# Optimization experiments

Hardware: AMD Instinct MI355X
Metric: run time of the kernel (lower is better)

Reference implementation:

```python
import jax, jax.numpy as jnp
import numpy as np

H = 12
DK = 64


def setup_inputs() -> dict:
    key = jax.random.key(0)
    ks = jax.random.split(key, 6)
    bs, ne, d = 32, 20, H * DK
    R = jax.random.normal(ks[0], (bs, ne, ne, d), dtype=jnp.float32)
    R_mas = jax.random.randint(ks[1], (bs, ne, ne, 1), 0, 2).astype(jnp.float32)
    WQ_w = jax.random.normal(ks[2], (DK, DK), dtype=jnp.float32) * (1.0 / np.sqrt(DK))
    WK_w = jax.random.normal(ks[3], (DK, DK), dtype=jnp.float32) * (1.0 / np.sqrt(DK))
    WV_w = jax.random.normal(ks[4], (DK, DK), dtype=jnp.float32) * (1.0 / np.sqrt(DK))
    zb = jnp.zeros((DK,), dtype=jnp.float32)
    return {"R": R, "R_mas": R_mas, "WQ_w": WQ_w, "WQ_b": zb, "WK_w": WK_w,
            "WK_b": zb, "WV_w": WV_w, "WV_b": zb}


def reference(R, R_mas, WQ_w, WQ_b, WK_w, WK_b, WV_w, WV_b):
    bs, ne, _, d = R.shape
    h, dk = H, DK
    n = ne * ne
    # (bs, h, ne, ne, dk)
    Rh = R.reshape(bs, ne, ne, h, dk).transpose(0, 3, 1, 2, 4)
    # per-head QKV linears (torch Linear: y = x @ W.T + b)
    Q = (Rh @ WQ_w.T + WQ_b).reshape(bs, h, n, dk)
    K = (Rh @ WK_w.T + WK_b).reshape(bs, h, n, dk)
    V = (Rh @ WV_w.T + WV_b).reshape(bs, h, n, dk)
    mas = R_mas.reshape(bs, 1, n)                      # (bs,1,n)
    att_mas = mas[:, :, :, None] * mas[:, :, None, :]  # (bs,1,n,n)
    alpha = jnp.einsum('bhqd,bhkd->bhqk', Q, K)        # (bs,h,n,n)
    alpha = alpha - (1.0 - att_mas) * 100000.0         # mask BEFORE scaling (faithful)
    alpha = jax.nn.softmax(alpha / jnp.sqrt(jnp.float32(dk)), axis=-1)
    R_Z = jnp.einsum('bhqk,bhkd->bhqd', alpha, V).reshape(bs, h, ne, ne, dk)
    R_Z = R_Z * R_mas.reshape(bs, 1, ne, ne, 1)
    # (bs, ne, ne, h*dk)
    return R_Z.transpose(0, 2, 3, 1, 4).reshape(bs, ne, ne, h * dk)
```

## Files before the change

kernel.cpp:

```cpp
#include <hip/hip_runtime.h>

typedef float    f32x4 __attribute__((ext_vector_type(4)));
typedef _Float16 f16x8 __attribute__((ext_vector_type(8)));
typedef _Float16 f16x4 __attribute__((ext_vector_type(4)));

#define MFMA16 __builtin_amdgcn_mfma_f32_16x16x32_f16

#define NQ     400
#define DMODEL 768

#define SCL 0.18033688011112042f
#define PEN 18033.688011112043f
#define M0  8.0f

#define K_OFF    0
#define VT_OFF   51200
#define W_OFF    105472
#define QS_OFF   130048
#define BIAS_OFF 162816
#define MKB_OFF  163584
#define SMEM_BYTES 163648

__device__ __forceinline__ f16x8 cvt8(const float* rp) {
    f32x4 u0 = *(const f32x4*)(rp);
    f32x4 u1 = *(const f32x4*)(rp + 4);
    f16x8 a;
    a[0] = (_Float16)u0[0]; a[1] = (_Float16)u0[1];
    a[2] = (_Float16)u0[2]; a[3] = (_Float16)u0[3];
    a[4] = (_Float16)u1[0]; a[5] = (_Float16)u1[1];
    a[6] = (_Float16)u1[2]; a[7] = (_Float16)u1[3];
    return a;
}

template <int M>
__device__ __forceinline__ void proj_kv(char* smem, f16x8 af0, f16x8 af1,
                                        int t, int g, int q16, int csw) {
    #pragma unroll
    for (int cg = 0; cg < 4; ++cg) {
        const int col = cg * 16 + q16;
        const float bb = *(const float*)(smem + BIAS_OFF + (M * 64 + col) * 4);
        f32x4 acc = {bb, bb, bb, bb};
        f16x8 wb0 = *(const f16x8*)(smem + W_OFF + M * 8192 + col * 128 + ((g * 16) ^ csw));
        f16x8 wb1 = *(const f16x8*)(smem + W_OFF + M * 8192 + col * 128 + ((64 + g * 16) ^ csw));
        acc = MFMA16(af0, wb0, acc, 0, 0, 0);
        acc = MFMA16(af1, wb1, acc, 0, 0, 0);
        if (M == 1) {
            #pragma unroll
            for (int r = 0; r < 4; ++r) {
                const int kk = t * 16 + 4 * g + r;
                *(_Float16*)(smem + K_OFF + kk * 128 + ((col * 2) ^ ((kk & 7) << 4))) =
                    (_Float16)acc[r];
            }
        } else {
            f16x4 hv;
            hv[0]=(_Float16)acc[0]; hv[1]=(_Float16)acc[1];
            hv[2]=(_Float16)acc[2]; hv[3]=(_Float16)acc[3];
            *(f16x4*)(smem + VT_OFF + col * 848 + (t >> 1) * 64 + g * 16 + (t & 1) * 8) = hv;
        }
    }
}

__global__ __launch_bounds__(1024, 4)
void attn_fused(const float* __restrict__ R, const float* __restrict__ Rmas,
                const float* __restrict__ Wq, const float* __restrict__ bq,
                const float* __restrict__ Wk, const float* __restrict__ bk,
                const float* __restrict__ Wv, const float* __restrict__ bv,
                float* __restrict__ out)
{
    extern __shared__ char smem[];
    const int tid  = threadIdx.x;
    const int lane = tid & 63;
    const int wv   = tid >> 6;
    const int g    = lane >> 4;
    const int q16  = lane & 15;
    const int csw  = (q16 & 7) << 4;

    const int blk  = blockIdx.x;
    const int b    = blk / 24;
    const int rem  = blk - b * 24;
    const int h    = rem >> 1;
    const int half = rem & 1;
    const int qlo   = half ? 13 : 0;
    const int ntile = half ? 12 : 13;

    {
        if (tid < 768) {
            const int m   = tid >> 8;
            const int idx = tid & 255;
            const int row = idx >> 2;
            const int c0  = (idx & 3) << 4;
            const float* Wm = (m == 0 ? Wq : (m == 1 ? Wk : Wv)) + row * 64 + c0;
            const int sw = (row & 7) << 4;
            #pragma unroll
            for (int k2 = 0; k2 < 2; ++k2) {
                f32x4 v0 = *(const f32x4*)(Wm + 8 * k2);
                f32x4 v1 = *(const f32x4*)(Wm + 8 * k2 + 4);
                f16x8 hv;
                hv[0]=(_Float16)v0[0]; hv[1]=(_Float16)v0[1];
                hv[2]=(_Float16)v0[2]; hv[3]=(_Float16)v0[3];
                hv[4]=(_Float16)v1[0]; hv[5]=(_Float16)v1[1];
                hv[6]=(_Float16)v1[2]; hv[7]=(_Float16)v1[3];
                *(f16x8*)(smem + W_OFF + m * 8192 + row * 128 + ((c0 * 2 + 16 * k2) ^ sw)) = hv;
            }
        } else if (tid < 960) {
            const int j = tid - 768;
            const float* bms[3] = {bq, bk, bv};
            *(float*)(smem + BIAS_OFF + j * 4) = bms[j >> 6][j & 63];
        }
        if (wv < 7) {
            const int i = (wv << 6) | lane;
            const float mval = (i < NQ) ? Rmas[b * NQ + i] : 0.0f;
            unsigned long long bb = __ballot(mval != 0.0f);
            if (lane == 0) {
                ((unsigned*)(smem + MKB_OFF))[2 * wv]     = (unsigned)bb;
                ((unsigned*)(smem + MKB_OFF))[2 * wv + 1] = (unsigned)(bb >> 32);
            }
        }
        if (tid < 256) {
            const int r = tid >> 2, c = tid & 3;
            *(f16x4*)(smem + VT_OFF + r * 848 + 768 + c * 16 + 8) = (f16x4){0, 0, 0, 0};
        }
    }
    __syncthreads();

    const float* Rbh = R + (size_t)b * NQ * DMODEL + h * 64;

    f16x8 qreg[2];
    const int QSw = QS_OFF + wv * 2048;
    if (wv < ntile) {
        const int t = qlo + wv;
        const float* rp = Rbh + (size_t)(t * 16 + q16) * DMODEL + g * 8;
        f16x8 af0 = cvt8(rp);
        f16x8 af1 = cvt8(rp + 32);
        #pragma unroll
        for (int cg = 0; cg < 4; ++cg) {
            const int col = cg * 16 + q16;
            const float bb = *(const float*)(smem + BIAS_OFF + col * 4);
            f32x4 acc = {bb, bb, bb, bb};
            f16x8 wb0 = *(const f16x8*)(smem + W_OFF + col * 128 + ((g * 16) ^ csw));
            f16x8 wb1 = *(const f16x8*)(smem + W_OFF + col * 128 + ((64 + g * 16) ^ csw));
            acc = MFMA16(af0, wb0, acc, 0, 0, 0);
            acc = MFMA16(af1, wb1, acc, 0, 0, 0);
            #pragma unroll
            for (int r = 0; r < 4; ++r) {
                const int rr = 4 * g + r;
                *(_Float16*)(smem + QSw + rr * 128 + ((col * 2) ^ ((rr & 7) << 4))) =
                    (_Float16)acc[r];
            }
        }
        proj_kv<1>(smem, af0, af1, t, g, q16, csw);
        proj_kv<2>(smem, af0, af1, t, g, q16, csw);
        asm volatile("s_waitcnt lgkmcnt(0)" ::: "memory");
        qreg[0] = *(const f16x8*)(smem + QSw + q16 * 128 + ((g * 16)      ^ csw));
        qreg[1] = *(const f16x8*)(smem + QSw + q16 * 128 + ((64 + g * 16) ^ csw));
    }
    {
        const int  t  = half ? (wv - 3) : (9 + wv);
        const bool ok = half ? (wv >= 3) : (wv >= 4);
        if (ok) {
            const float* rp = Rbh + (size_t)(t * 16 + q16) * DMODEL + g * 8;
            f16x8 af0 = cvt8(rp);
            f16x8 af1 = cvt8(rp + 32);
            proj_kv<1>(smem, af0, af1, t, g, q16, csw);
            proj_kv<2>(smem, af0, af1, t, g, q16, csw);
        }
    }
    if (wv == 0) {
        #pragma unroll
        for (int i = 0; i < 7; ++i) {
            const int k = i * 64 + lane;
            if (k < NQ) {
                const unsigned bit =
                    (((const unsigned*)(smem + MKB_OFF))[k >> 5] >> (k & 31)) & 1u;
                *(float*)(smem + QS_OFF + k * 4) = bit ? -M0 : -(M0 + PEN);
            }
        }
    }
    __syncthreads();

    if (wv < ntile) {
        const int qt   = qlo + wv;
        const int qrow = qt * 16 + q16;
        const unsigned qb = (((const unsigned*)(smem + MKB_OFF))[qrow >> 5] >> (qrow & 31)) & 1u;

        const int kbase = K_OFF + q16 * 128;
        const int o0 = (g * 16) ^ csw;
        const int o1 = (64 + g * 16) ^ csw;

        f32x4 oc[4];
        #pragma unroll
        for (int cg = 0; cg < 4; ++cg) oc[cg] = (f32x4){0.f, 0.f, 0.f, 0.f};
        float ps = 0.f;

        f16x8 ka0 = *(const f16x8*)(smem + kbase + o0);
        f16x8 ka1 = *(const f16x8*)(smem + kbase + o1);

        #pragma unroll 1
        for (int kc = 0; kc < 12; ++kc) {
            const char* kb_base = smem + kbase + kc * 4096 + 2048;
            f16x8 kb0 = *(const f16x8*)(kb_base + o0);
            f16x8 kb1 = *(const f16x8*)(kb_base + o1);
            f32x4 pa4 = *(const f32x4*)(smem + QS_OFF + (kc * 32 + 4 * g) * 4);
            f32x4 pb4 = *(const f32x4*)(smem + QS_OFF + (kc * 32 + 16 + 4 * g) * 4);

            f32x4 accA = {0.f, 0.f, 0.f, 0.f};
            accA = MFMA16(ka0, qreg[0], accA, 0, 0, 0);
            accA = MFMA16(ka1, qreg[1], accA, 0, 0, 0);
            f32x4 accB = {0.f, 0.f, 0.f, 0.f};
            accB = MFMA16(kb0, qreg[0], accB, 0, 0, 0);
            accB = MFMA16(kb1, qreg[1], accB, 0, 0, 0);

            const char* kn_base = smem + kbase + (kc + 1) * 4096;
            ka0 = *(const f16x8*)(kn_base + o0);
            ka1 = *(const f16x8*)(kn_base + o1);

            f16x4 pha, phb;
            #pragma unroll
            for (int r = 0; r < 4; ++r) {
                const float e = __builtin_amdgcn_exp2f(fmaf(accA[r], SCL, pa4[r]));
                ps += e;
                pha[r] = (_Float16)e;
            }
            #pragma unroll
            for (int r = 0; r < 4; ++r) {
                const float e = __builtin_amdgcn_exp2f(fmaf(accB[r], SCL, pb4[r]));
                ps += e;
                phb[r] = (_Float16)e;
            }
            union { f16x4 hh[2]; f16x8 v; } pu;
            pu.hh[0] = pha;
            pu.hh[1] = phb;
            const f16x8 pa = pu.v;
            #pragma unroll
            for (int cg = 0; cg < 4; ++cg) {
                f16x8 vb = *(const f16x8*)(smem + VT_OFF + (cg * 16 + q16) * 848 + kc * 64 + g * 16);
                oc[cg] = MFMA16(pa, vb, oc[cg], 0, 0, 0);
            }
        }
        {
            f32x4 pa4 = *(const f32x4*)(smem + QS_OFF + (384 + 4 * g) * 4);
            f32x4 accA = {0.f, 0.f, 0.f, 0.f};
            accA = MFMA16(ka0, qreg[0], accA, 0, 0, 0);
            accA = MFMA16(ka1, qreg[1], accA, 0, 0, 0);
            f16x4 pha;
            #pragma unroll
            for (int r = 0; r < 4; ++r) {
                const float e = __builtin_amdgcn_exp2f(fmaf(accA[r], SCL, pa4[r]));
                ps += e;
                pha[r] = (_Float16)e;
            }
            union { f16x4 hh[2]; f16x8 v; } pu;
            pu.hh[0] = pha;
            pu.hh[1] = (f16x4){0, 0, 0, 0};
            const f16x8 pa = pu.v;
            #pragma unroll
            for (int cg = 0; cg < 4; ++cg) {
                f16x8 vb = *(const f16x8*)(smem + VT_OFF + (cg * 16 + q16) * 848 + 12 * 64 + g * 16);
                oc[cg] = MFMA16(pa, vb, oc[cg], 0, 0, 0);
            }
        }

        ps += __shfl_xor(ps, 16);
        ps += __shfl_xor(ps, 32);
        const float myrs = qb ? __builtin_amdgcn_rcpf(ps) : 0.0f;

        float rs[4];
        #pragma unroll
        for (int r = 0; r < 4; ++r) rs[r] = __shfl(myrs, 4 * g + r);
        float* op = out + (size_t)(b * NQ + qt * 16) * DMODEL + h * 64;
        #pragma unroll
        for (int r = 0; r < 4; ++r) {
            #pragma unroll
            for (int cg = 0; cg < 4; ++cg)
                op[(4 * g + r) * DMODEL + cg * 16 + q16] = oc[cg][r] * rs[r];
        }
    }
}

extern "C" void kernel_launch(void* const* d_in, const int* in_sizes, int n_in,
                              void* d_out, int out_size, void* d_ws, size_t ws_size,
                              hipStream_t stream) {
    const float* R    = (const float*)d_in[0];
    const float* Rmas = (const float*)d_in[1];
    const float* Wq   = (const float*)d_in[2];
    const float* bq   = (const float*)d_in[3];
    const float* Wk   = (const float*)d_in[4];
    const float* bk   = (const float*)d_in[5];
    const float* Wv   = (const float*)d_in[6];
    const float* bv   = (const float*)d_in[7];
    float* out = (float*)d_out;

    (void)hipFuncSetAttribute(reinterpret_cast<const void*>(attn_fused),
                              hipFuncAttributeMaxDynamicSharedMemorySize, SMEM_BYTES);
    attn_fused<<<dim3(768), dim3(1024), SMEM_BYTES, stream>>>(R, Rmas, Wq, bq, Wk, bk, Wv, bv, out);
}
```

Baseline: 49.05 us.

## Compute Q transposed in registers, pack f16 conversions, prefetch K fully

The Q projection now swaps the MFMA operand order so the output lands directly in the register layout the attention loop needs. This removes the Q staging through shared memory and the wait on it. The K projection is transposed the same way so it writes packed f16x4 stores instead of scalar halves. Float-to-half conversions use the packed round-toward-zero instruction, which lowers the conversion instruction count but rounds slightly differently. Both K fragments for the next chunk are now prefetched one iteration ahead, and shared memory shrinks by the removed Q scratch.

```diff
diff --git a/kernel.cpp b/kernel.cpp
--- a/kernel.cpp
+++ b/kernel.cpp
@@ -3,8 +3,18 @@
 typedef float    f32x4 __attribute__((ext_vector_type(4)));
 typedef _Float16 f16x8 __attribute__((ext_vector_type(8)));
 typedef _Float16 f16x4 __attribute__((ext_vector_type(4)));
+typedef _Float16 f16x2 __attribute__((ext_vector_type(2)));
+typedef __fp16   fp16x2_raw __attribute__((ext_vector_type(2)));
 
 #define MFMA16 __builtin_amdgcn_mfma_f32_16x16x32_f16
+
+__device__ __forceinline__ f16x2 pkrtz(float a, float b) {
+    fp16x2_raw t = __builtin_amdgcn_cvt_pkrtz(a, b);
+    union { fp16x2_raw r; f16x2 h; } u;
+    u.r = t;
+    return u.h;
+}
+#define PKRTZ pkrtz
 
 #define NQ     400
 #define DMODEL 768
@@ -13,51 +23,86 @@
 #define PEN 18033.688011112043f
 #define M0  8.0f
 
+
 #define K_OFF    0
 #define VT_OFF   51200
 #define W_OFF    105472
-#define QS_OFF   130048
-#define BIAS_OFF 162816
-#define MKB_OFF  163584
-#define SMEM_BYTES 163648
+#define PEN_OFF  130048
+#define BIAS_OFF 131648
+#define MKB_OFF  132416
+#define SMEM_BYTES 132480
 
 __device__ __forceinline__ f16x8 cvt8(const float* rp) {
     f32x4 u0 = *(const f32x4*)(rp);
     f32x4 u1 = *(const f32x4*)(rp + 4);
-    f16x8 a;
-    a[0] = (_Float16)u0[0]; a[1] = (_Float16)u0[1];
-    a[2] = (_Float16)u0[2]; a[3] = (_Float16)u0[3];
-    a[4] = (_Float16)u1[0]; a[5] = (_Float16)u1[1];
-    a[6] = (_Float16)u1[2]; a[7] = (_Float16)u1[3];
-    return a;
-}
-
-template <int M>
-__device__ __forceinline__ void proj_kv(char* smem, f16x8 af0, f16x8 af1,
-                                        int t, int g, int q16, int csw) {
+    union { f16x2 h2[4]; f16x8 v; } u;
+    u.h2[0] = PKRTZ(u0[0], u0[1]);
+    u.h2[1] = PKRTZ(u0[2], u0[3]);
+    u.h2[2] = PKRTZ(u1[0], u1[1]);
+    u.h2[3] = PKRTZ(u1[2], u1[3]);
+    return u.v;
+}
+
+__device__ __forceinline__ void proj_v(char* smem, f16x8 af0, f16x8 af1,
+                                       int t, int g, int q16, int csw) {
     #pragma unroll
     for (int cg = 0; cg < 4; ++cg) {
         const int col = cg * 16 + q16;
-        const float bb = *(const float*)(smem + BIAS_OFF + (M * 64 + col) * 4);
+        const float bb = *(const float*)(smem + BIAS_OFF + (128 + col) * 4);
         f32x4 acc = {bb, bb, bb, bb};
-        f16x8 wb0 = *(const f16x8*)(smem + W_OFF + M * 8192 + col * 128 + ((g * 16) ^ csw));
-        f16x8 wb1 = *(const f16x8*)(smem + W_OFF + M * 8192 + col * 128 + ((64 + g * 16) ^ csw));
+        f16x8 wb0 = *(const f16x8*)(smem + W_OFF + 16384 + col * 128 + ((g * 16) ^ csw));
+        f16x8 wb1 = *(const f16x8*)(smem + W_OFF + 16384 + col * 128 + ((64 + g * 16) ^ csw));
         acc = MFMA16(af0, wb0, acc, 0, 0, 0);
         acc = MFMA16(af1, wb1, acc, 0, 0, 0);
-        if (M == 1) {
-            #pragma unroll
-            for (int r = 0; r < 4; ++r) {
-                const int kk = t * 16 + 4 * g + r;
-                *(_Float16*)(smem + K_OFF + kk * 128 + ((col * 2) ^ ((kk & 7) << 4))) =
-                    (_Float16)acc[r];
-            }
-        } else {
-            f16x4 hv;
-            hv[0]=(_Float16)acc[0]; hv[1]=(_Float16)acc[1];
-            hv[2]=(_Float16)acc[2]; hv[3]=(_Float16)acc[3];
-            *(f16x4*)(smem + VT_OFF + col * 848 + (t >> 1) * 64 + g * 16 + (t & 1) * 8) = hv;
-        }
-    }
+        union { f16x2 h2[2]; f16x4 v; } hv;
+        hv.h2[0] = PKRTZ(acc[0], acc[1]);
+        hv.h2[1] = PKRTZ(acc[2], acc[3]);
+        *(f16x4*)(smem + VT_OFF + col * 848 + (t >> 1) * 64 + g * 16 + (t & 1) * 8) = hv.v;
+    }
+}
+
+__device__ __forceinline__ void proj_k(char* smem, f16x8 af0, f16x8 af1,
+                                       int kk, int g, int q16, int csw) {
+    #pragma unroll
+    for (int cg = 0; cg < 4; ++cg) {
+        const int d0 = cg * 16 + 4 * g;
+        f32x4 acc = *(const f32x4*)(smem + BIAS_OFF + (64 + d0) * 4);
+        f16x8 wb0 = *(const f16x8*)(smem + W_OFF + 8192 + (cg * 16 + q16) * 128 + ((g * 16) ^ csw));
+        f16x8 wb1 = *(const f16x8*)(smem + W_OFF + 8192 + (cg * 16 + q16) * 128 + ((64 + g * 16) ^ csw));
+        acc = MFMA16(wb0, af0, acc, 0, 0, 0);
+        acc = MFMA16(wb1, af1, acc, 0, 0, 0);
+        union { f16x2 h2[2]; f16x4 v; } hv;
+        hv.h2[0] = PKRTZ(acc[0], acc[1]);
+        hv.h2[1] = PKRTZ(acc[2], acc[3]);
+        const int pos2 = ((cg & 2) << 5) + g * 16 + (cg & 1) * 8;
+        *(f16x4*)(smem + K_OFF + kk * 128 + (pos2 ^ csw)) = hv.v;
+    }
+}
+
+__device__ __forceinline__ void proj_q(char* smem, f16x8 af0, f16x8 af1,
+                                       int g, int q16, int csw, f16x8 (&qreg)[2]) {
+    f32x4 qa[4];
+    #pragma unroll
+    for (int cg = 0; cg < 4; ++cg) {
+        const int d0 = cg * 16 + 4 * g;
+        f32x4 acc = *(const f32x4*)(smem + BIAS_OFF + d0 * 4);
+        f16x8 wb0 = *(const f16x8*)(smem + W_OFF + (cg * 16 + q16) * 128 + ((g * 16) ^ csw));
+        f16x8 wb1 = *(const f16x8*)(smem + W_OFF + (cg * 16 + q16) * 128 + ((64 + g * 16) ^ csw));
+        acc = MFMA16(wb0, af0, acc, 0, 0, 0);
+        acc = MFMA16(wb1, af1, acc, 0, 0, 0);
+        qa[cg] = acc;
+    }
+    union { f16x2 h2[4]; f16x8 v; } u0, u1;
+    u0.h2[0] = PKRTZ(qa[0][0], qa[0][1]);
+    u0.h2[1] = PKRTZ(qa[0][2], qa[0][3]);
+    u0.h2[2] = PKRTZ(qa[1][0], qa[1][1]);
+    u0.h2[3] = PKRTZ(qa[1][2], qa[1][3]);
+    u1.h2[0] = PKRTZ(qa[2][0], qa[2][1]);
+    u1.h2[1] = PKRTZ(qa[2][2], qa[2][3]);
+    u1.h2[2] = PKRTZ(qa[3][0], qa[3][1]);
+    u1.h2[3] = PKRTZ(qa[3][2], qa[3][3]);
+    qreg[0] = u0.v;
+    qreg[1] = u1.v;
 }
 
 __global__ __launch_bounds__(1024, 4)
@@ -95,12 +140,12 @@
             for (int k2 = 0; k2 < 2; ++k2) {
                 f32x4 v0 = *(const f32x4*)(Wm + 8 * k2);
                 f32x4 v1 = *(const f32x4*)(Wm + 8 * k2 + 4);
-                f16x8 hv;
-                hv[0]=(_Float16)v0[0]; hv[1]=(_Float16)v0[1];
-                hv[2]=(_Float16)v0[2]; hv[3]=(_Float16)v0[3];
-                hv[4]=(_Float16)v1[0]; hv[5]=(_Float16)v1[1];
-                hv[6]=(_Float16)v1[2]; hv[7]=(_Float16)v1[3];
-                *(f16x8*)(smem + W_OFF + m * 8192 + row * 128 + ((c0 * 2 + 16 * k2) ^ sw)) = hv;
+                union { f16x2 h2[4]; f16x8 v; } hv;
+                hv.h2[0] = PKRTZ(v0[0], v0[1]);
+                hv.h2[1] = PKRTZ(v0[2], v0[3]);
+                hv.h2[2] = PKRTZ(v1[0], v1[1]);
+                hv.h2[3] = PKRTZ(v1[2], v1[3]);
+                *(f16x8*)(smem + W_OFF + m * 8192 + row * 128 + ((c0 * 2 + 16 * k2) ^ sw)) = hv.v;
             }
         } else if (tid < 960) {
             const int j = tid - 768;
@@ -126,33 +171,14 @@
     const float* Rbh = R + (size_t)b * NQ * DMODEL + h * 64;
 
     f16x8 qreg[2];
-    const int QSw = QS_OFF + wv * 2048;
     if (wv < ntile) {
         const int t = qlo + wv;
         const float* rp = Rbh + (size_t)(t * 16 + q16) * DMODEL + g * 8;
         f16x8 af0 = cvt8(rp);
         f16x8 af1 = cvt8(rp + 32);
-        #pragma unroll
-        for (int cg = 0; cg < 4; ++cg) {
-            const int col = cg * 16 + q16;
-            const float bb = *(const float*)(smem + BIAS_OFF + col * 4);
-            f32x4 acc = {bb, bb, bb, bb};
-            f16x8 wb0 = *(const f16x8*)(smem + W_OFF + col * 128 + ((g * 16) ^ csw));
-            f16x8 wb1 = *(const f16x8*)(smem + W_OFF + col * 128 + ((64 + g * 16) ^ csw));
-            acc = MFMA16(af0, wb0, acc, 0, 0, 0);
-            acc = MFMA16(af1, wb1, acc, 0, 0, 0);
-            #pragma unroll
-            for (int r = 0; r < 4; ++r) {
-                const int rr = 4 * g + r;
-                *(_Float16*)(smem + QSw + rr * 128 + ((col * 2) ^ ((rr & 7) << 4))) =
-                    (_Float16)acc[r];
-            }
-        }
-        proj_kv<1>(smem, af0, af1, t, g, q16, csw);
-        proj_kv<2>(smem, af0, af1, t, g, q16, csw);
-        asm volatile("s_waitcnt lgkmcnt(0)" ::: "memory");
-        qreg[0] = *(const f16x8*)(smem + QSw + q16 * 128 + ((g * 16)      ^ csw));
-        qreg[1] = *(const f16x8*)(smem + QSw + q16 * 128 + ((64 + g * 16) ^ csw));
+        proj_q(smem, af0, af1, g, q16, csw, qreg);
+        proj_k(smem, af0, af1, t * 16 + q16, g, q16, csw);
+        proj_v(smem, af0, af1, t, g, q16, csw);
     }
     {
         const int  t  = half ? (wv - 3) : (9 + wv);
@@ -161,8 +187,8 @@
             const float* rp = Rbh + (size_t)(t * 16 + q16) * DMODEL + g * 8;
             f16x8 af0 = cvt8(rp);
             f16x8 af1 = cvt8(rp + 32);
-            proj_kv<1>(smem, af0, af1, t, g, q16, csw);
-            proj_kv<2>(smem, af0, af1, t, g, q16, csw);
+            proj_k(smem, af0, af1, t * 16 + q16, g, q16, csw);
+            proj_v(smem, af0, af1, t, g, q16, csw);
         }
     }
     if (wv == 0) {
@@ -172,7 +198,7 @@
             if (k < NQ) {
                 const unsigned bit =
                     (((const unsigned*)(smem + MKB_OFF))[k >> 5] >> (k & 31)) & 1u;
-                *(float*)(smem + QS_OFF + k * 4) = bit ? -M0 : -(M0 + PEN);
+                *(float*)(smem + PEN_OFF + k * 4) = bit ? -M0 : -(M0 + PEN);
             }
         }
     }
@@ -194,14 +220,13 @@
 
         f16x8 ka0 = *(const f16x8*)(smem + kbase + o0);
         f16x8 ka1 = *(const f16x8*)(smem + kbase + o1);
+        f16x8 kb0 = *(const f16x8*)(smem + kbase + 2048 + o0);
+        f16x8 kb1 = *(const f16x8*)(smem + kbase + 2048 + o1);
 
         #pragma unroll 1
         for (int kc = 0; kc < 12; ++kc) {
-            const char* kb_base = smem + kbase + kc * 4096 + 2048;
-            f16x8 kb0 = *(const f16x8*)(kb_base + o0);
-            f16x8 kb1 = *(const f16x8*)(kb_base + o1);
-            f32x4 pa4 = *(const f32x4*)(smem + QS_OFF + (kc * 32 + 4 * g) * 4);
-            f32x4 pb4 = *(const f32x4*)(smem + QS_OFF + (kc * 32 + 16 + 4 * g) * 4);
+            f32x4 pa4 = *(const f32x4*)(smem + PEN_OFF + (kc * 32 + 4 * g) * 4);
+            f32x4 pb4 = *(const f32x4*)(smem + PEN_OFF + (kc * 32 + 16 + 4 * g) * 4);
 
             f32x4 accA = {0.f, 0.f, 0.f, 0.f};
             accA = MFMA16(ka0, qreg[0], accA, 0, 0, 0);
@@ -210,26 +235,27 @@
             accB = MFMA16(kb0, qreg[0], accB, 0, 0, 0);
             accB = MFMA16(kb1, qreg[1], accB, 0, 0, 0);
 
-            const char* kn_base = smem + kbase + (kc + 1) * 4096;
-            ka0 = *(const f16x8*)(kn_base + o0);
-            ka1 = *(const f16x8*)(kn_base + o1);
-
-            f16x4 pha, phb;
-            #pragma unroll
-            for (int r = 0; r < 4; ++r) {
-                const float e = __builtin_amdgcn_exp2f(fmaf(accA[r], SCL, pa4[r]));
-                ps += e;
-                pha[r] = (_Float16)e;
-            }
-            #pragma unroll
-            for (int r = 0; r < 4; ++r) {
-                const float e = __builtin_amdgcn_exp2f(fmaf(accB[r], SCL, pb4[r]));
-                ps += e;
-                phb[r] = (_Float16)e;
-            }
-            union { f16x4 hh[2]; f16x8 v; } pu;
-            pu.hh[0] = pha;
-            pu.hh[1] = phb;
+            const char* kn = smem + kbase + (kc + 1) * 4096;
+            ka0 = *(const f16x8*)(kn + o0);
+            ka1 = *(const f16x8*)(kn + o1);
+            kb0 = *(const f16x8*)(kn + 2048 + o0);
+            kb1 = *(const f16x8*)(kn + 2048 + o1);
+
+            const float e0 = __builtin_amdgcn_exp2f(fmaf(accA[0], SCL, pa4[0]));
+            const float e1 = __builtin_amdgcn_exp2f(fmaf(accA[1], SCL, pa4[1]));
+            const float e2 = __builtin_amdgcn_exp2f(fmaf(accA[2], SCL, pa4[2]));
+            const float e3 = __builtin_amdgcn_exp2f(fmaf(accA[3], SCL, pa4[3]));
+            const float e4 = __builtin_amdgcn_exp2f(fmaf(accB[0], SCL, pb4[0]));
+            const float e5 = __builtin_amdgcn_exp2f(fmaf(accB[1], SCL, pb4[1]));
+            const float e6 = __builtin_amdgcn_exp2f(fmaf(accB[2], SCL, pb4[2]));
+            const float e7 = __builtin_amdgcn_exp2f(fmaf(accB[3], SCL, pb4[3]));
+            ps += ((e0 + e1) + (e2 + e3)) + ((e4 + e5) + (e6 + e7));
+
+            union { f16x2 h2[4]; f16x8 v; } pu;
+            pu.h2[0] = PKRTZ(e0, e1);
+            pu.h2[1] = PKRTZ(e2, e3);
+            pu.h2[2] = PKRTZ(e4, e5);
+            pu.h2[3] = PKRTZ(e6, e7);
             const f16x8 pa = pu.v;
             #pragma unroll
             for (int cg = 0; cg < 4; ++cg) {
@@ -238,20 +264,20 @@
             }
         }
         {
-            f32x4 pa4 = *(const f32x4*)(smem + QS_OFF + (384 + 4 * g) * 4);
+            f32x4 pa4 = *(const f32x4*)(smem + PEN_OFF + (384 + 4 * g) * 4);
             f32x4 accA = {0.f, 0.f, 0.f, 0.f};
             accA = MFMA16(ka0, qreg[0], accA, 0, 0, 0);
             accA = MFMA16(ka1, qreg[1], accA, 0, 0, 0);
-            f16x4 pha;
-            #pragma unroll
-            for (int r = 0; r < 4; ++r) {
-                const float e = __builtin_amdgcn_exp2f(fmaf(accA[r], SCL, pa4[r]));
-                ps += e;
-                pha[r] = (_Float16)e;
-            }
-            union { f16x4 hh[2]; f16x8 v; } pu;
-            pu.hh[0] = pha;
-            pu.hh[1] = (f16x4){0, 0, 0, 0};
+            const float e0 = __builtin_amdgcn_exp2f(fmaf(accA[0], SCL, pa4[0]));
+            const float e1 = __builtin_amdgcn_exp2f(fmaf(accA[1], SCL, pa4[1]));
+            const float e2 = __builtin_amdgcn_exp2f(fmaf(accA[2], SCL, pa4[2]));
+            const float e3 = __builtin_amdgcn_exp2f(fmaf(accA[3], SCL, pa4[3]));
+            ps += (e0 + e1) + (e2 + e3);
+            union { f16x2 h2[4]; f16x8 v; } pu;
+            pu.h2[0] = PKRTZ(e0, e1);
+            pu.h2[1] = PKRTZ(e2, e3);
+            pu.h2[2] = (f16x2){0, 0};
+            pu.h2[3] = (f16x2){0, 0};
             const f16x8 pa = pu.v;
             #pragma unroll
             for (int cg = 0; cg < 4; ++cg) {
```

Result: faster. 47.97 us (-2.2%).
